# Kernel tuning notes

Hardware: AMD Instinct MI355X
Metric: run time of the kernel (lower is better)

The kernel has to match this reference:

```python
import jax, jax.numpy as jnp
import numpy as np

N = 100000
E = 1600000
D_IN = 64
D_OUT = 64

def setup_inputs() -> dict:
    key = jax.random.key(0)
    k1, k2, k3 = jax.random.split(key, 3)
    x = jax.random.normal(k1, (N, D_IN), dtype=jnp.float32)
    edge_index = jax.random.randint(k2, (2, E), 0, N, dtype=jnp.int32)
    W = jax.random.normal(k3, (D_IN, D_OUT), dtype=jnp.float32) * (1.0 / np.sqrt(D_IN))
    b = jnp.zeros((D_OUT,), dtype=jnp.float32)
    return {"x": x, "edge_index": edge_index, "W": W, "b": b}

def reference(x, edge_index, W, b):
    # GCN.forward in eval mode: dropout is identity; GCNConv with
    # normalize=True, add_self_loops=True, edge_weight=None (all ones).
    loop = jnp.arange(N, dtype=edge_index.dtype)
    row = jnp.concatenate([edge_index[0], loop])   # source nodes, [E+N]
    col = jnp.concatenate([edge_index[1], loop])   # target nodes, [E+N]
    ew = jnp.ones(row.shape[0], dtype=x.dtype)
    # symmetric normalization: deg over targets, norm = d^-1/2[row] * d^-1/2[col]
    deg = jax.ops.segment_sum(ew, col, num_segments=N)
    dinv = jnp.where(deg > 0, jax.lax.rsqrt(deg), 0.0)
    norm = dinv[row] * dinv[col]                   # [E+N]
    h = x @ W                                      # [N, D_OUT] dense GEMM first (PyG order)
    msg = h[row] * norm[:, None]                   # gather + scale, [E+N, D_OUT]
    out = jax.ops.segment_sum(msg, col, num_segments=N)  # scatter-add aggregate
    return out + b
```

## Files before the change

kernel.cpp:

```cpp
#include <hip/hip_runtime.h>
#include <hip/hip_fp16.h>
#include <math.h>

constexpr int D = 64;
constexpr int BNODES = 128;
constexpr int BSHIFT = 7;
constexpr int BSTRIDE = 3072;
constexpr int PCHUNK = 4096;
constexpr int NB_MAX = 1024;

typedef _Float16 half8 __attribute__((ext_vector_type(8)));
typedef float floatx4 __attribute__((ext_vector_type(4)));

__global__ __launch_bounds__(256) void k_init(const float* __restrict__ W,
                                              __half* __restrict__ Wt,
                                              int* __restrict__ bcur, int NB) {
    const int i = blockIdx.x * 256 + threadIdx.x;
    if (i < NB) bcur[i] = i * BSTRIDE;
    if (i < D * D) {
        const int j = i >> 6;
        const int k = i & 63;
        Wt[i] = __float2half(W[k * D + j]);
    }
}

__global__ __launch_bounds__(512) void k_partition(
        const int* __restrict__ ei, int* __restrict__ bcur,
        unsigned* __restrict__ ebuf, int E, int NB) {
    __shared__ int lh[NB_MAX];
    __shared__ int lb[NB_MAX];
    __shared__ int cc[PCHUNK];
    const int t = threadIdx.x;
    for (int j = t; j < NB; j += 512) lh[j] = 0;
    __syncthreads();
    const int e0 = blockIdx.x * PCHUNK;
    const int e1 = min(e0 + PCHUNK, E);
    const bool full = (e1 - e0 == PCHUNK);

    if (full) {
        const int4* cp = reinterpret_cast<const int4*>(ei + E + e0);
        const int4 ca = cp[t];
        const int4 cb = cp[t + 512];
        reinterpret_cast<int4*>(cc)[t]       = ca;
        reinterpret_cast<int4*>(cc)[t + 512] = cb;
        atomicAdd(&lh[ca.x >> BSHIFT], 1); atomicAdd(&lh[ca.y >> BSHIFT], 1);
        atomicAdd(&lh[ca.z >> BSHIFT], 1); atomicAdd(&lh[ca.w >> BSHIFT], 1);
        atomicAdd(&lh[cb.x >> BSHIFT], 1); atomicAdd(&lh[cb.y >> BSHIFT], 1);
        atomicAdd(&lh[cb.z >> BSHIFT], 1); atomicAdd(&lh[cb.w >> BSHIFT], 1);
    } else {
        for (int e = e0 + t; e < e1; e += 512) {
            const int c = ei[E + e];
            cc[e - e0] = c;
            atomicAdd(&lh[c >> BSHIFT], 1);
        }
    }
    __syncthreads();
    for (int j = t; j < NB; j += 512) {
        const int n = lh[j];
        lb[j] = n ? atomicAdd(&bcur[j], n) : 0;
        lh[j] = 0;
    }
    __syncthreads();

    if (full) {
        const int4* rp = reinterpret_cast<const int4*>(ei + e0);
        const int4 ra = rp[t];
        const int4 rb = rp[t + 512];
        const int r8[8] = {ra.x, ra.y, ra.z, ra.w, rb.x, rb.y, rb.z, rb.w};
#pragma unroll
        for (int k = 0; k < 8; ++k) {
            const int ci = (k < 4) ? (4 * t + k) : (2048 + 4 * t + (k - 4));
            const int c = cc[ci];
            const int bkt = c >> BSHIFT;
            const int rank = atomicAdd(&lh[bkt], 1);
            const int pos = lb[bkt] + rank;
            if (pos < (bkt + 1) * BSTRIDE)
                ebuf[pos] = ((unsigned)r8[k] << BSHIFT) | (unsigned)(c & (BNODES - 1));
        }
    } else {
        for (int e = e0 + t; e < e1; e += 512) {
            const int r = ei[e];
            const int c = cc[e - e0];
            const int bkt = c >> BSHIFT;
            const int rank = atomicAdd(&lh[bkt], 1);
            const int pos = lb[bkt] + rank;
            if (pos < (bkt + 1) * BSTRIDE)
                ebuf[pos] = ((unsigned)r << BSHIFT) | (unsigned)(c & (BNODES - 1));
        }
    }
}

__global__ __launch_bounds__(512) void k_gemm_fused(
        const float* __restrict__ x, const __half* __restrict__ Wt,
        const unsigned* __restrict__ ebuf, const int* __restrict__ bcur,
        __half* __restrict__ gh0, __half* __restrict__ gh1, int N) {
    __shared__ int lh[BNODES];
    const int j = blockIdx.x;
    const int t = threadIdx.x;
    const int base = j << BSHIFT;
    const int s0 = j * BSTRIDE;
    const int s1 = min(bcur[j], s0 + BSTRIDE);

    if (t < BNODES) lh[t] = 0;
    __syncthreads();
    for (int i = s0 + t; i < s1; i += 512)
        atomicAdd(&lh[ebuf[i] & (BNODES - 1)], 1);
    __syncthreads();

    const int wave = t >> 6;
    const int node16 = base + wave * 16;
    if (node16 >= N) return;
    const int lane = t & 63;
    const int r16  = lane & 15;
    const int kq   = lane >> 4;

    const _Float16* wt = (const _Float16*)Wt;
    half8 bf[4][2];
#pragma unroll
    for (int jt = 0; jt < 4; ++jt)
#pragma unroll
        for (int s = 0; s < 2; ++s)
            bf[jt][s] = *(const half8*)(wt + (jt * 16 + r16) * D + s * 32 + kq * 8);

    half8 af[2];
#pragma unroll
    for (int s = 0; s < 2; ++s) {
        const float4* xp = reinterpret_cast<const float4*>(
            x + (size_t)(node16 + r16) * D + s * 32 + kq * 8);
        const float4 x0 = xp[0];
        const float4 x1 = xp[1];
        half8 a;
        a[0] = (_Float16)x0.x; a[1] = (_Float16)x0.y;
        a[2] = (_Float16)x0.z; a[3] = (_Float16)x0.w;
        a[4] = (_Float16)x1.x; a[5] = (_Float16)x1.y;
        a[6] = (_Float16)x1.z; a[7] = (_Float16)x1.w;
        af[s] = a;
    }

    floatx4 acc[4];
#pragma unroll
    for (int jt = 0; jt < 4; ++jt) {
        acc[jt] = (floatx4){0.f, 0.f, 0.f, 0.f};
        acc[jt] = __builtin_amdgcn_mfma_f32_16x16x32_f16(af[0], bf[jt][0], acc[jt], 0, 0, 0);
        acc[jt] = __builtin_amdgcn_mfma_f32_16x16x32_f16(af[1], bf[jt][1], acc[jt], 0, 0, 0);
    }

#pragma unroll
    for (int r = 0; r < 4; ++r) {
        const int nl = wave * 16 + kq * 4 + r;
        const int node = base + nl;
        const float dinv = rsqrtf((float)(lh[nl] + 1));
#pragma unroll
        for (int jt = 0; jt < 2; ++jt)
            gh0[(size_t)node * 32 + jt * 16 + r16] = __float2half(acc[jt][r] * dinv);
#pragma unroll
        for (int jt = 2; jt < 4; ++jt)
            gh1[(size_t)node * 32 + (jt - 2) * 16 + r16] = __float2half(acc[jt][r] * dinv);
    }
}

__global__ __launch_bounds__(512) void k_breduce(
        const unsigned* __restrict__ ebuf, const int* __restrict__ bcur,
        const __half* __restrict__ gh0, const __half* __restrict__ gh1,
        const float* __restrict__ b, float* __restrict__ out, int N) {
    __shared__ int srcLDS[BSTRIDE];
    __shared__ int lh[BNODES];
    __shared__ int st[BNODES];
    __shared__ int lcur[BNODES];
    const int j = blockIdx.x;
    const int t = threadIdx.x;
    const int s0 = j * BSTRIDE;
    const int s1 = min(bcur[j], s0 + BSTRIDE);
    const int base = j << BSHIFT;
    const int nn = min(BNODES, N - base);

    if (t < BNODES) lh[t] = 0;
    __syncthreads();
    for (int i = s0 + t; i < s1; i += 512)
        atomicAdd(&lh[ebuf[i] & (BNODES - 1)], 1);
    __syncthreads();
    if (t < BNODES) st[t] = lh[t];
    __syncthreads();
    for (int off = 1; off < BNODES; off <<= 1) {
        int y = 0;
        if (t < BNODES && t >= off) y = st[t - off];
        __syncthreads();
        if (t < BNODES && t >= off) st[t] += y;
        __syncthreads();
    }
    if (t < BNODES) {
        const int s = st[t] - lh[t];
        st[t] = s;
        lcur[t] = s;
    }
    __syncthreads();
    for (int i = s0 + t; i < s1; i += 512) {
        const unsigned code = ebuf[i];
        const int c = code & (BNODES - 1);
        const int rank = atomicAdd(&lcur[c], 1);
        srcLDS[rank] = (int)(code >> BSHIFT);
    }
    __syncthreads();

    const int g  = t >> 2;
    const int fl = t & 3;
    if (g >= nn) return;

    const int node = base + g;
    const int start = st[g];
    const int num = lh[g];
    const float dinv = rsqrtf((float)(num + 1));
    const float4* b4 = reinterpret_cast<const float4*>(b);
    float4* o4 = reinterpret_cast<float4*>(out);
    const __half2 z = __float2half2_rn(0.f);

#pragma unroll
    for (int phase = 0; phase < 2; ++phase) {
        const uint4* gp = reinterpret_cast<const uint4*>(phase ? gh1 : gh0);

        const uint4 su = gp[(size_t)node * 4 + fl];
        __half2 a0 = *(const __half2*)&su.x;
        __half2 a1 = *(const __half2*)&su.y;
        __half2 a2 = *(const __half2*)&su.z;
        __half2 a3 = *(const __half2*)&su.w;
        __half2 c0 = z, c1 = z, c2 = z, c3 = z;

        int i = start;
        const int end = start + num;
        for (; i + 2 <= end; i += 2) {
            const int r0 = srcLDS[i];
            const int r1 = srcLDS[i + 1];
            const uint4 u0 = gp[(size_t)r0 * 4 + fl];
            const uint4 u1 = gp[(size_t)r1 * 4 + fl];
            a0 = __hadd2(a0, *(const __half2*)&u0.x);
            a1 = __hadd2(a1, *(const __half2*)&u0.y);
            a2 = __hadd2(a2, *(const __half2*)&u0.z);
            a3 = __hadd2(a3, *(const __half2*)&u0.w);
            c0 = __hadd2(c0, *(const __half2*)&u1.x);
            c1 = __hadd2(c1, *(const __half2*)&u1.y);
            c2 = __hadd2(c2, *(const __half2*)&u1.z);
            c3 = __hadd2(c3, *(const __half2*)&u1.w);
        }
        if (i < end) {
            const int r = srcLDS[i];
            const uint4 u = gp[(size_t)r * 4 + fl];
            a0 = __hadd2(a0, *(const __half2*)&u.x);
            a1 = __hadd2(a1, *(const __half2*)&u.y);
            a2 = __hadd2(a2, *(const __half2*)&u.z);
            a3 = __hadd2(a3, *(const __half2*)&u.w);
        }
        a0 = __hadd2(a0, c0);
        a1 = __hadd2(a1, c1);
        a2 = __hadd2(a2, c2);
        a3 = __hadd2(a3, c3);

        const float2 f0 = __half22float2(a0);
        const float2 f1 = __half22float2(a1);
        const float2 f2 = __half22float2(a2);
        const float2 f3 = __half22float2(a3);
        const int ob = phase * 8 + fl * 2;
        const float4 bb0 = b4[ob];
        const float4 bb1 = b4[ob + 1];
        float4 o0, o1;
        o0.x = fmaf(dinv, f0.x, bb0.x); o0.y = fmaf(dinv, f0.y, bb0.y);
        o0.z = fmaf(dinv, f1.x, bb0.z); o0.w = fmaf(dinv, f1.y, bb0.w);
        o1.x = fmaf(dinv, f2.x, bb1.x); o1.y = fmaf(dinv, f2.y, bb1.y);
        o1.z = fmaf(dinv, f3.x, bb1.z); o1.w = fmaf(dinv, f3.y, bb1.w);
        o4[(size_t)node * 16 + ob]     = o0;
        o4[(size_t)node * 16 + ob + 1] = o1;
    }
}

extern "C" void kernel_launch(void* const* d_in, const int* in_sizes, int n_in,
                              void* d_out, int out_size, void* d_ws, size_t ws_size,
                              hipStream_t stream) {
    const float* x  = (const float*)d_in[0];
    const int*   ei = (const int*)d_in[1];
    const float* W  = (const float*)d_in[2];
    const float* b  = (const float*)d_in[3];
    float* out = (float*)d_out;

    const int N = in_sizes[0] / D;
    const int E = in_sizes[1] / 2;
    const int NB = (N + BNODES - 1) >> BSHIFT;
    const int blocksP = (E + PCHUNK - 1) / PCHUNK;

    __half*   gh0  = (__half*)d_ws;
    __half*   gh1  = gh0 + (size_t)N * 32;
    __half*   Wt   = gh1 + (size_t)N * 32;
    unsigned* ebuf = (unsigned*)(Wt + D * D);
    int*      bcur = (int*)(ebuf + (size_t)NB * BSTRIDE);

    k_init      <<<16, 256, 0, stream>>>(W, Wt, bcur, NB);
    k_partition <<<blocksP, 512, 0, stream>>>(ei, bcur, ebuf, E, NB);
    k_gemm_fused<<<NB, 512, 0, stream>>>(x, Wt, ebuf, bcur, gh0, gh1, N);
    k_breduce   <<<NB, 512, 0, stream>>>(ebuf, bcur, gh0, gh1, b, out, N);
}
```

Measured before the change: 88.98 us.

## Merge split half-feature buffers into one row layout and widen gather

Replaces the two 32-column fp16 buffers with a single 64-column row-major buffer. Each gathered neighbour row becomes one contiguous 128-byte read by 8 lanes, instead of two separate 64-byte reads done in two phases. The reduce kernel now gives each 8-lane group two nodes, unrolls the neighbour loop by four with independent accumulators, and computes the LDS prefix scan with wave shuffles instead of a barrier-heavy loop. Fewer, wider random gathers and more memory-level parallelism should help, at the cost of more registers per thread.

```diff
diff --git a/kernel.cpp b/kernel.cpp
--- a/kernel.cpp
+++ b/kernel.cpp
@@ -93,7 +93,7 @@
 __global__ __launch_bounds__(512) void k_gemm_fused(
         const float* __restrict__ x, const __half* __restrict__ Wt,
         const unsigned* __restrict__ ebuf, const int* __restrict__ bcur,
-        __half* __restrict__ gh0, __half* __restrict__ gh1, int N) {
+        __half* __restrict__ gh, int N) {
     __shared__ int lh[BNODES];
     const int j = blockIdx.x;
     const int t = threadIdx.x;
@@ -151,18 +151,15 @@
         const int node = base + nl;
         const float dinv = rsqrtf((float)(lh[nl] + 1));
 #pragma unroll
-        for (int jt = 0; jt < 2; ++jt)
-            gh0[(size_t)node * 32 + jt * 16 + r16] = __float2half(acc[jt][r] * dinv);
-#pragma unroll
-        for (int jt = 2; jt < 4; ++jt)
-            gh1[(size_t)node * 32 + (jt - 2) * 16 + r16] = __float2half(acc[jt][r] * dinv);
+        for (int jt = 0; jt < 4; ++jt)
+            gh[(size_t)node * D + jt * 16 + r16] = __float2half(acc[jt][r] * dinv);
     }
 }
 
 __global__ __launch_bounds__(512) void k_breduce(
         const unsigned* __restrict__ ebuf, const int* __restrict__ bcur,
-        const __half* __restrict__ gh0, const __half* __restrict__ gh1,
-        const float* __restrict__ b, float* __restrict__ out, int N) {
+        const __half* __restrict__ gh, const float* __restrict__ b,
+        float* __restrict__ out, int N) {
     __shared__ int srcLDS[BSTRIDE];
     __shared__ int lh[BNODES];
     __shared__ int st[BNODES];
@@ -179,19 +176,18 @@
     for (int i = s0 + t; i < s1; i += 512)
         atomicAdd(&lh[ebuf[i] & (BNODES - 1)], 1);
     __syncthreads();
-    if (t < BNODES) st[t] = lh[t];
-    __syncthreads();
-    for (int off = 1; off < BNODES; off <<= 1) {
-        int y = 0;
-        if (t < BNODES && t >= off) y = st[t - off];
-        __syncthreads();
-        if (t < BNODES && t >= off) st[t] += y;
-        __syncthreads();
-    }
-    if (t < BNODES) {
-        const int s = st[t] - lh[t];
-        st[t] = s;
-        lcur[t] = s;
+    if (t < 64) {
+        const int v0 = lh[2 * t];
+        const int v1 = lh[2 * t + 1];
+        int s = v0 + v1;
+#pragma unroll
+        for (int off = 1; off < 64; off <<= 1) {
+            const int y = __shfl_up(s, off, 64);
+            if (t >= off) s += y;
+        }
+        const int excl = s - (v0 + v1);
+        st[2 * t] = excl;         st[2 * t + 1] = excl + v0;
+        lcur[2 * t] = excl;       lcur[2 * t + 1] = excl + v0;
     }
     __syncthreads();
     for (int i = s0 + t; i < s1; i += 512) {
@@ -202,72 +198,84 @@
     }
     __syncthreads();
 
-    const int g  = t >> 2;
-    const int fl = t & 3;
-    if (g >= nn) return;
-
-    const int node = base + g;
-    const int start = st[g];
-    const int num = lh[g];
-    const float dinv = rsqrtf((float)(num + 1));
+    const int g8 = t >> 3;
+    const int fl = t & 7;
+
+    const uint4* g4 = reinterpret_cast<const uint4*>(gh);
     const float4* b4 = reinterpret_cast<const float4*>(b);
     float4* o4 = reinterpret_cast<float4*>(out);
     const __half2 z = __float2half2_rn(0.f);
-
-#pragma unroll
-    for (int phase = 0; phase < 2; ++phase) {
-        const uint4* gp = reinterpret_cast<const uint4*>(phase ? gh1 : gh0);
-
-        const uint4 su = gp[(size_t)node * 4 + fl];
-        __half2 a0 = *(const __half2*)&su.x;
-        __half2 a1 = *(const __half2*)&su.y;
-        __half2 a2 = *(const __half2*)&su.z;
-        __half2 a3 = *(const __half2*)&su.w;
-        __half2 c0 = z, c1 = z, c2 = z, c3 = z;
+    const float4 bb0 = b4[fl * 2];
+    const float4 bb1 = b4[fl * 2 + 1];
+
+#pragma unroll
+    for (int q = 0; q < 2; ++q) {
+        const int nl = q * 64 + g8;
+        if (nl >= nn) continue;
+        const int node = base + nl;
+        const int start = st[nl];
+        const int num = lh[nl];
+
+        const uint4 su = g4[(size_t)node * 8 + fl];
+        __half2 a0 = *(const __half2*)&su.x, a1 = *(const __half2*)&su.y;
+        __half2 a2 = *(const __half2*)&su.z, a3 = *(const __half2*)&su.w;
+        __half2 p0 = z, p1 = z, p2 = z, p3 = z;
+        __half2 q0 = z, q1 = z, q2 = z, q3 = z;
+        __half2 s0h = z, s1h = z, s2h = z, s3h = z;
 
         int i = start;
         const int end = start + num;
-        for (; i + 2 <= end; i += 2) {
+        for (; i + 4 <= end; i += 4) {
             const int r0 = srcLDS[i];
             const int r1 = srcLDS[i + 1];
-            const uint4 u0 = gp[(size_t)r0 * 4 + fl];
-            const uint4 u1 = gp[(size_t)r1 * 4 + fl];
+            const int r2 = srcLDS[i + 2];
+            const int r3 = srcLDS[i + 3];
+            const uint4 u0 = g4[(size_t)r0 * 8 + fl];
+            const uint4 u1 = g4[(size_t)r1 * 8 + fl];
+            const uint4 u2 = g4[(size_t)r2 * 8 + fl];
+            const uint4 u3 = g4[(size_t)r3 * 8 + fl];
             a0 = __hadd2(a0, *(const __half2*)&u0.x);
             a1 = __hadd2(a1, *(const __half2*)&u0.y);
             a2 = __hadd2(a2, *(const __half2*)&u0.z);
             a3 = __hadd2(a3, *(const __half2*)&u0.w);
-            c0 = __hadd2(c0, *(const __half2*)&u1.x);
-            c1 = __hadd2(c1, *(const __half2*)&u1.y);
-            c2 = __hadd2(c2, *(const __half2*)&u1.z);
-            c3 = __hadd2(c3, *(const __half2*)&u1.w);
-        }
-        if (i < end) {
+            p0 = __hadd2(p0, *(const __half2*)&u1.x);
+            p1 = __hadd2(p1, *(const __half2*)&u1.y);
+            p2 = __hadd2(p2, *(const __half2*)&u1.z);
+            p3 = __hadd2(p3, *(const __half2*)&u1.w);
+            q0 = __hadd2(q0, *(const __half2*)&u2.x);
+            q1 = __hadd2(q1, *(const __half2*)&u2.y);
+            q2 = __hadd2(q2, *(const __half2*)&u2.z);
+            q3 = __hadd2(q3, *(const __half2*)&u2.w);
+            s0h = __hadd2(s0h, *(const __half2*)&u3.x);
+            s1h = __hadd2(s1h, *(const __half2*)&u3.y);
+            s2h = __hadd2(s2h, *(const __half2*)&u3.z);
+            s3h = __hadd2(s3h, *(const __half2*)&u3.w);
+        }
+        for (; i < end; ++i) {
             const int r = srcLDS[i];
-            const uint4 u = gp[(size_t)r * 4 + fl];
+            const uint4 u = g4[(size_t)r * 8 + fl];
             a0 = __hadd2(a0, *(const __half2*)&u.x);
             a1 = __hadd2(a1, *(const __half2*)&u.y);
             a2 = __hadd2(a2, *(const __half2*)&u.z);
             a3 = __hadd2(a3, *(const __half2*)&u.w);
         }
-        a0 = __hadd2(a0, c0);
-        a1 = __hadd2(a1, c1);
-        a2 = __hadd2(a2, c2);
-        a3 = __hadd2(a3, c3);
-
+        a0 = __hadd2(__hadd2(a0, p0), __hadd2(q0, s0h));
+        a1 = __hadd2(__hadd2(a1, p1), __hadd2(q1, s1h));
+        a2 = __hadd2(__hadd2(a2, p2), __hadd2(q2, s2h));
+        a3 = __hadd2(__hadd2(a3, p3), __hadd2(q3, s3h));
+
+        const float dinv = rsqrtf((float)(num + 1));
         const float2 f0 = __half22float2(a0);
         const float2 f1 = __half22float2(a1);
         const float2 f2 = __half22float2(a2);
         const float2 f3 = __half22float2(a3);
-        const int ob = phase * 8 + fl * 2;
-        const float4 bb0 = b4[ob];
-        const float4 bb1 = b4[ob + 1];
         float4 o0, o1;
         o0.x = fmaf(dinv, f0.x, bb0.x); o0.y = fmaf(dinv, f0.y, bb0.y);
         o0.z = fmaf(dinv, f1.x, bb0.z); o0.w = fmaf(dinv, f1.y, bb0.w);
         o1.x = fmaf(dinv, f2.x, bb1.x); o1.y = fmaf(dinv, f2.y, bb1.y);
         o1.z = fmaf(dinv, f3.x, bb1.z); o1.w = fmaf(dinv, f3.y, bb1.w);
-        o4[(size_t)node * 16 + ob]     = o0;
-        o4[(size_t)node * 16 + ob + 1] = o1;
+        o4[(size_t)node * 16 + fl * 2]     = o0;
+        o4[(size_t)node * 16 + fl * 2 + 1] = o1;
     }
 }
 
@@ -285,14 +293,13 @@
     const int NB = (N + BNODES - 1) >> BSHIFT;
     const int blocksP = (E + PCHUNK - 1) / PCHUNK;
 
-    __half*   gh0  = (__half*)d_ws;
-    __half*   gh1  = gh0 + (size_t)N * 32;
-    __half*   Wt   = gh1 + (size_t)N * 32;
+    __half*   gh   = (__half*)d_ws;
+    __half*   Wt   = gh + (size_t)N * D;
     unsigned* ebuf = (unsigned*)(Wt + D * D);
     int*      bcur = (int*)(ebuf + (size_t)NB * BSTRIDE);
 
     k_init      <<<16, 256, 0, stream>>>(W, Wt, bcur, NB);
     k_partition <<<blocksP, 512, 0, stream>>>(ei, bcur, ebuf, E, NB);
-    k_gemm_fused<<<NB, 512, 0, stream>>>(x, Wt, ebuf, bcur, gh0, gh1, N);
-    k_breduce   <<<NB, 512, 0, stream>>>(ebuf, bcur, gh0, gh1, b, out, N);
-}
+    k_gemm_fused<<<NB, 512, 0, stream>>>(x, Wt, ebuf, bcur, gh, N);
+    k_breduce   <<<NB, 512, 0, stream>>>(ebuf, bcur, gh, b, out, N);
+}
```

Result: faster. 78.95 us, median of 2 (-11.3%).
